# Optimization experiments

Measured on AMD Instinct MI355X. Metric: run time of the kernel, lower is better.

## Reference

```python
import jax, jax.numpy as jnp
import numpy as np

DIM = 128; NH = 4; WS = 7; SS = 3
ZP, HP, WP = 14, 56, 56
NMLP = 512; EPS = 1e-5
N = WS ** 3  # tokens per window (343)


def _ln(x, g, b):
    m = x.mean(-1, keepdims=True)
    v = x.var(-1, keepdims=True)
    return (x - m) / jnp.sqrt(v + EPS) * g + b


def _rel_index():
    # static relative-position index for a cubic (WS,WS,WS) window
    c = np.stack(np.meshgrid(np.arange(WS), np.arange(WS), np.arange(WS), indexing='ij')).reshape(3, -1)
    rel = (c[:, :, None] - c[:, None, :]).transpose(1, 2, 0) + (WS - 1)
    rel[..., 0] *= (2 * WS - 1) ** 2
    rel[..., 1] *= (2 * WS - 1)
    return rel.sum(-1).reshape(-1)  # [N*N]


def _attn_mask():
    # static shifted-window attention mask, [nW, N, N]
    img = np.zeros((ZP, HP, WP), np.float32)
    cnt = 0
    sl = (slice(0, -WS), slice(-WS, -SS), slice(-SS, None))
    for z in sl:
        for h in sl:
            for w in sl:
                img[z, h, w] = cnt
                cnt += 1
    m = img.reshape(ZP // WS, WS, HP // WS, WS, WP // WS, WS)
    m = m.transpose(0, 2, 4, 1, 3, 5).reshape(-1, N)
    d = m[:, None, :] - m[:, :, None]
    return np.where(d != 0, np.float32(-100.0), np.float32(0.0))


_REL_IDX = jnp.asarray(_rel_index())
_MASK = jnp.asarray(_attn_mask())


def setup_inputs() -> dict:
    key = jax.random.key(0)
    ks = jax.random.split(key, 8)
    return {
        'x': jax.random.normal(ks[0], (2, ZP, HP, WP, DIM), jnp.float32),
        'norm1_g': jnp.ones((DIM,), jnp.float32),
        'norm1_b': jnp.zeros((DIM,), jnp.float32),
        'qkv_w': jax.random.normal(ks[1], (DIM, 3 * DIM), jnp.float32) * 0.02,
        'qkv_b': jnp.zeros((3 * DIM,), jnp.float32),
        'rel_table': jax.random.normal(ks[2], ((2 * WS - 1) ** 3, NH), jnp.float32) * 0.02,
        'proj_w': jax.random.normal(ks[3], (DIM, DIM), jnp.float32) * 0.02,
        'proj_b': jnp.zeros((DIM,), jnp.float32),
        'norm2_g': jnp.ones((DIM,), jnp.float32),
        'norm2_b': jnp.zeros((DIM,), jnp.float32),
        'fc1_w': jax.random.normal(ks[4], (DIM, NMLP), jnp.float32) * 0.02,
        'fc1_b': jnp.zeros((NMLP,), jnp.float32),
        'fc2_w': jax.random.normal(ks[5], (NMLP, DIM), jnp.float32) * 0.02,
        'fc2_b': jnp.zeros((DIM,), jnp.float32),
    }


def reference(x, norm1_g, norm1_b, qkv_w, qkv_b, rel_table, proj_w, proj_b,
              norm2_g, norm2_b, fc1_w, fc1_b, fc2_w, fc2_b):
    B, Z, H, W, C = x.shape
    hd = C // NH
    scale = hd ** -0.5
    shortcut = x
    xn = _ln(x, norm1_g, norm1_b)
    # cyclic shift
    xs = jnp.roll(xn, (-SS, -SS, -SS), axis=(1, 2, 3))
    # window partition -> [B*nW, N, C]
    xw = xs.reshape(B, Z // WS, WS, H // WS, WS, W // WS, WS, C)
    xw = xw.transpose(0, 1, 3, 5, 2, 4, 6, 7).reshape(-1, N, C)
    qkv = (xw @ qkv_w + qkv_b).reshape(-1, N, 3, NH, hd).transpose(2, 0, 3, 1, 4)
    q, k, v = qkv[0], qkv[1], qkv[2]  # [Bn, NH, N, hd]
    attn = jnp.einsum('bhnd,bhmd->bhnm', q * scale, k)
    bias = rel_table[_REL_IDX].reshape(N, N, NH).transpose(2, 0, 1)  # [NH, N, N]
    attn = attn + bias[None]
    nW = _MASK.shape[0]
    attn = attn.reshape(B, nW, NH, N, N) + _MASK[None, :, None]
    attn = jax.nn.softmax(attn.reshape(-1, NH, N, N), axis=-1)
    out = jnp.einsum('bhnm,bhmd->bhnd', attn, v)
    out = out.transpose(0, 2, 1, 3).reshape(-1, N, C)
    out = out @ proj_w + proj_b
    # window reverse -> [B, Z, H, W, C]
    out = out.reshape(B, Z // WS, H // WS, W // WS, WS, WS, WS, C)
    out = out.transpose(0, 1, 4, 2, 5, 3, 6, 7).reshape(B, Z, H, W, C)
    out = jnp.roll(out, (SS, SS, SS), axis=(1, 2, 3))
    x1 = shortcut + out
    y = _ln(x1, norm2_g, norm2_b)
    y = jax.nn.gelu(y @ fc1_w + fc1_b, approximate=False) @ fc2_w + fc2_b
    return x1 + y
```

## Files before the change

### kernel.cpp

```cpp
#include <hip/hip_runtime.h>


typedef __attribute__((ext_vector_type(8))) _Float16 half8;
typedef __attribute__((ext_vector_type(4))) _Float16 half4;
typedef __attribute__((ext_vector_type(4))) float floatx4;

#define DEV static __device__ __forceinline__

DEV floatx4 MFMA(half8 a, half8 b, floatx4 c) {
  return __builtin_amdgcn_mfma_f32_16x16x32_f16(a, b, c, 0, 0, 0);
}
DEV floatx4 MFMA16(half4 a, half4 b, floatx4 c) {
  return __builtin_amdgcn_mfma_f32_16x16x16f16(a, b, c, 0, 0, 0);
}

DEV float gelu_f(float v) {
  return v / (1.f + __expf(-1.702f * v));
}

DEV void f4arr(float4 v, float o[4]) {
  o[0] = v.x; o[1] = v.y; o[2] = v.z; o[3] = v.w;
}

DEV void stage_load(half8 pf[8], const _Float16* src, int rst, int tid) {
#pragma unroll
  for (int it = 0; it < 8; ++it) {
    int e = it * 256 + tid;
    int row = e >> 4, seg = e & 15;
    pf[it] = *(const half8*)&src[(size_t)row * rst + seg * 8];
  }
}
DEV void stage_store(_Float16* wb, const half8 pf[8], int tid) {
#pragma unroll
  for (int it = 0; it < 8; ++it) {
    int e = it * 256 + tid;
    int row = e >> 4, seg = e & 15;
    *(half8*)&wb[row * 136 + seg * 8] = pf[it];
  }
}
DEV void stage_tile(_Float16* wb, const _Float16* src, int rst, int tid) {
  half8 pf[8];
  stage_load(pf, src, rst, tid);
  stage_store(wb, pf, tid);
}

__global__ __launch_bounds__(256) void k_prep(
    const float* __restrict__ rel, _Float16* __restrict__ biasH,
    const float* __restrict__ w1, const float* __restrict__ w2,
    const float* __restrict__ wq, const float* __restrict__ wp,
    _Float16* __restrict__ w1h, _Float16* __restrict__ w2h,
    _Float16* __restrict__ wqh, _Float16* __restrict__ wph) {
  int gid = blockIdx.x * 256 + threadIdx.x;
  if (gid < 495616) {
    int reg = gid & 3, quad = (gid >> 2) & 3, ml = (gid >> 4) & 15;
    int u = gid >> 8;
    int nt = u % 22; u /= 22;
    int rt = u % 22; int h = u / 22;
    int q = rt * 16 + ml, kv = nt * 16 + quad * 4 + reg;
    float val = -30000.f;
    if (q < 343 && kv < 343) {
      int lzi = q / 49, ri = q - lzi * 49, lhi = ri / 7, lwi = ri - lhi * 7;
      int lzj = kv / 49, rj = kv - lzj * 49, lhj = rj / 7, lwj = rj - lhj * 7;
      int idx = (lzi - lzj + 6) * 169 + (lhi - lhj + 6) * 13 + (lwi - lwj + 6);
      val = rel[idx * 4 + h];
    }
    biasH[gid] = (_Float16)val;
    return;
  }
  int i = gid - 495616;
  if (i < 65536) {
    int n = i >> 7, k = i & 127;
    w1h[i] = (_Float16)w1[k * 512 + n];
  } else if (i < 131072) {
    int j = i - 65536; int n = j >> 9, k = j & 511;
    w2h[j] = (_Float16)w2[k * 128 + n];
  } else if (i < 180224) {
    int j = i - 131072; int n = j >> 7, k = j & 127;
    wqh[j] = (_Float16)wq[k * 384 + n];
  } else if (i < 196608) {
    int j = i - 180224; int n = j >> 7, k = j & 127;
    wph[j] = (_Float16)wp[k * 128 + n];
  }
}

__global__ __launch_bounds__(256) void k_ln_qkv(
    const float* __restrict__ x, const float* __restrict__ g1,
    const float* __restrict__ b1, const _Float16* __restrict__ wqh,
    const float* __restrict__ bq, _Float16* __restrict__ qkv) {
  __shared__ __align__(16) _Float16 wb[128 * 136];
  const int tid = threadIdx.x, lane = tid & 63, wid = tid >> 6;
  const int ml = lane & 15, quad = lane >> 4;
  const int task = blockIdx.x * 4 + wid;
  const int w = task / 11, pr = task - (task / 11) * 11;
  const int b_ = w >> 7, r = w & 127;
  const int wz = r >> 6, wh = (r >> 3) & 7, ww = r & 7;

  half8 a0[4], a1[4];
#pragma unroll
  for (int hf = 0; hf < 2; ++hf) {
    int t = pr * 32 + hf * 16 + ml; if (t > 342) t = 342;
    int lz = t / 49, rr = t - lz * 49, lh = rr / 7, lw = rr - lh * 7;
    int oz = wz * 7 + lz + 3; if (oz >= 14) oz -= 14;
    int oh = wh * 7 + lh + 3; if (oh >= 56) oh -= 56;
    int ow = ww * 7 + lw + 3; if (ow >= 56) ow -= 56;
    const float* xp = x + ((((b_ * 14 + oz) * 56 + oh) * 56 + ow) << 7);
    float xv[32];
    float s = 0.f, ss = 0.f;
#pragma unroll
    for (int ks = 0; ks < 4; ++ks) {
      float4 p0 = *(const float4*)(xp + ks * 32 + quad * 8);
      float4 p1 = *(const float4*)(xp + ks * 32 + quad * 8 + 4);
      xv[ks * 8 + 0] = p0.x; xv[ks * 8 + 1] = p0.y; xv[ks * 8 + 2] = p0.z; xv[ks * 8 + 3] = p0.w;
      xv[ks * 8 + 4] = p1.x; xv[ks * 8 + 5] = p1.y; xv[ks * 8 + 6] = p1.z; xv[ks * 8 + 7] = p1.w;
      s += (p0.x + p0.y) + (p0.z + p0.w) + (p1.x + p1.y) + (p1.z + p1.w);
      ss += (p0.x * p0.x + p0.y * p0.y) + (p0.z * p0.z + p0.w * p0.w) +
            (p1.x * p1.x + p1.y * p1.y) + (p1.z * p1.z + p1.w * p1.w);
    }
    s += __shfl_xor(s, 16); s += __shfl_xor(s, 32);
    ss += __shfl_xor(ss, 16); ss += __shfl_xor(ss, 32);
    float mean = s * 0.0078125f;
    float rstd = rsqrtf(ss * 0.0078125f - mean * mean + 1e-5f);
#pragma unroll
    for (int ks = 0; ks < 4; ++ks) {
      int k0 = ks * 32 + quad * 8;
      float4 gg0 = *(const float4*)(g1 + k0), gg1 = *(const float4*)(g1 + k0 + 4);
      float4 bb0 = *(const float4*)(b1 + k0), bb1 = *(const float4*)(b1 + k0 + 4);
      half8 a;
      a[0] = (_Float16)((xv[ks * 8 + 0] - mean) * rstd * gg0.x + bb0.x);
      a[1] = (_Float16)((xv[ks * 8 + 1] - mean) * rstd * gg0.y + bb0.y);
      a[2] = (_Float16)((xv[ks * 8 + 2] - mean) * rstd * gg0.z + bb0.z);
      a[3] = (_Float16)((xv[ks * 8 + 3] - mean) * rstd * gg0.w + bb0.w);
      a[4] = (_Float16)((xv[ks * 8 + 4] - mean) * rstd * gg1.x + bb1.x);
      a[5] = (_Float16)((xv[ks * 8 + 5] - mean) * rstd * gg1.y + bb1.y);
      a[6] = (_Float16)((xv[ks * 8 + 6] - mean) * rstd * gg1.z + bb1.z);
      a[7] = (_Float16)((xv[ks * 8 + 7] - mean) * rstd * gg1.w + bb1.w);
      if (hf == 0) a0[ks] = a; else a1[ks] = a;
    }
  }

  const int t0 = pr * 32 + ml;
  const int t1 = t0 + 16;
  _Float16* q0 = qkv + ((size_t)w * 343 + t0) * 384;
  _Float16* q1 = qkv + ((size_t)w * 343 + (t1 < 343 ? t1 : 342)) * 384;

  for (int c = 0; c < 3; ++c) {
    __syncthreads();
    stage_tile(wb, wqh + (size_t)c * 128 * 128, 128, tid);
    __syncthreads();
    for (int ntl = 0; ntl < 8; ++ntl) {
      floatx4 acc0 = {0.f, 0.f, 0.f, 0.f}, acc1 = {0.f, 0.f, 0.f, 0.f};
#pragma unroll
      for (int ks = 0; ks < 4; ++ks) {
        half8 bb = *(const half8*)&wb[(ntl * 16 + ml) * 136 + ks * 32 + quad * 8];
        acc0 = MFMA(bb, a0[ks], acc0);
        acc1 = MFMA(bb, a1[ks], acc1);
      }
      const int colb = c * 128 + ntl * 16 + quad * 4;
      float qb[4]; f4arr(*(const float4*)&bq[colb], qb);
      half4 s0, s1;
#pragma unroll
      for (int reg = 0; reg < 4; ++reg) {
        s0[reg] = (_Float16)(acc0[reg] + qb[reg]);
        s1[reg] = (_Float16)(acc1[reg] + qb[reg]);
      }
      *(half4*)&q0[colb] = s0;
      if (t1 < 343) *(half4*)&q1[colb] = s1;
    }
  }
}

__global__ __launch_bounds__(512, 2) void k_attn(const _Float16* __restrict__ qkv,
                                                 const _Float16* __restrict__ biasH,
                                                 _Float16* __restrict__ aout) {
  __shared__ __align__(16) _Float16 kl[352 * 40];
  __shared__ __align__(16) _Float16 vt[32 * 364];
  __shared__ __align__(16) _Float16 pen[27 * 360];
  __shared__ __align__(4) unsigned char region[352];
  const int tid = threadIdx.x;
  const int w = blockIdx.x >> 2, head = blockIdx.x & 3;
  const int r = w & 127;
  const int wz = r >> 6, wh = (r >> 3) & 7, ww = r & 7;
  const bool fz = (wz == 1), fh = (wh == 7), fw = (ww == 7);

  for (int t = tid; t < 352; t += 512) {
    int rg = 255;
    if (t < 343) {
      int lz = t / 49, rr = t - lz * 49, lh = rr / 7, lw = rr - lh * 7;
      int rz = fz ? (lz < 4 ? 1 : 2) : 0;
      int rh2 = fh ? (lh < 4 ? 1 : 2) : 0;
      int rw2 = fw ? (lw < 4 ? 1 : 2) : 0;
      rg = rz * 9 + rh2 * 3 + rw2;
    }
    region[t] = (unsigned char)rg;
  }
  for (int e = tid; e < 27 * 352; e += 512) {
    int rg = e / 352, t = e - rg * 352;
    int rt_ = 255;
    if (t < 343) {
      int lz = t / 49, rr = t - lz * 49, lh = rr / 7, lw = rr - lh * 7;
      int rz = fz ? (lz < 4 ? 1 : 2) : 0;
      int rh2 = fh ? (lh < 4 ? 1 : 2) : 0;
      int rw2 = fw ? (lw < 4 ? 1 : 2) : 0;
      rt_ = rz * 9 + rh2 * 3 + rw2;
    }
    pen[rg * 360 + t] = (rt_ == rg) ? (_Float16)0.f : (_Float16)(-30000.f);
  }
  const _Float16* qkvw = qkv + (size_t)w * 343 * 384;
  for (int e = tid; e < 352 * 4; e += 512) {
    int t = e >> 2, d8 = (e & 3) * 8;
    half8 v;
    if (t < 343) {
      v = *(const half8*)&qkvw[t * 384 + 128 + head * 32 + d8];
    } else {
#pragma unroll
      for (int j = 0; j < 8; ++j) v[j] = (_Float16)0.f;
    }
    *(half8*)&kl[t * 40 + d8] = v;
  }
  for (int e = tid; e < 343 * 4; e += 512) {
    int t = e >> 2, d8 = (e & 3) * 8;
    half8 v = *(const half8*)&qkvw[t * 384 + 256 + head * 32 + d8];
#pragma unroll
    for (int j = 0; j < 8; ++j) vt[(d8 + j) * 364 + t] = v[j];
  }
  for (int e = tid; e < 9 * 32; e += 512) {
    int t = 343 + (e >> 5), d = e & 31;
    vt[d * 364 + t] = (_Float16)0.f;
  }
  __syncthreads();

  const int lane = tid & 63, wid = tid >> 6;
  const int ml = lane & 15, quad = lane >> 4;
  const float scale = 0.17677669529663687f;

  for (int rt = wid; rt < 22; rt += 8) {
    const int row0 = rt * 16;
    int qrow = row0 + ml; if (qrow > 342) qrow = 342;
    half8 bq8 = *(const half8*)&qkvw[qrow * 384 + head * 32 + quad * 8];
    const int rq = region[qrow];
    const _Float16* penr = &pen[rq * 360 + quad * 4];
    const _Float16* bb = &biasH[(size_t)((head * 22 + rt) * 22) * 256 + ml * 16 + quad * 4];

    floatx4 o0 = {0.f, 0.f, 0.f, 0.f}, o1 = {0.f, 0.f, 0.f, 0.f};
    floatx4 sm4 = {0.f, 0.f, 0.f, 0.f};
#pragma unroll
    for (int g = 0; g < 3; ++g) {
      const int G = (g < 2) ? 8 : 6;
      const int nb = g * 8;
      half4 bp[8];
      floatx4 S[8];
#pragma unroll
      for (int k = 0; k < 8; ++k) if (k < G) {
        half4 b4 = *(const half4*)&bb[(nb + k) * 256];
        half4 p4 = *(const half4*)&penr[(nb + k) * 16];
        bp[k] = b4 + p4;
      }
#pragma unroll
      for (int k = 0; k < 8; ++k) if (k < G) {
        half8 ak = *(const half8*)&kl[((nb + k) * 16 + ml) * 40 + quad * 8];
        S[k] = MFMA(ak, bq8, (floatx4){0.f, 0.f, 0.f, 0.f});
      }
#pragma unroll
      for (int k = 0; k < 8; ++k) if (k < G) {
        half4 p;
#pragma unroll
        for (int reg = 0; reg < 4; ++reg) {
          float v = fmaf(S[k][reg], scale, (float)bp[k][reg]);
          float e = __expf(v);
          sm4[reg] += e;
          p[reg] = (_Float16)e;
        }
        half4 va0 = *(const half4*)&vt[ml * 364 + (nb + k) * 16 + quad * 4];
        half4 va1 = *(const half4*)&vt[(16 + ml) * 364 + (nb + k) * 16 + quad * 4];
        o0 = MFMA16(va0, p, o0);
        o1 = MFMA16(va1, p, o1);
      }
    }
    float sm = (sm4[0] + sm4[1]) + (sm4[2] + sm4[3]);
    sm += __shfl_xor(sm, 16);
    sm += __shfl_xor(sm, 32);

    const int orow = row0 + ml;
    if (orow < 343) {
      float inv = 1.f / sm;
      _Float16* op = aout + ((size_t)w * 343 + orow) * 128 + head * 32;
      half4 s0, s1;
#pragma unroll
      for (int reg = 0; reg < 4; ++reg) {
        s0[reg] = (_Float16)(o0[reg] * inv);
        s1[reg] = (_Float16)(o1[reg] * inv);
      }
      *(half4*)&op[quad * 4] = s0;
      *(half4*)&op[16 + quad * 4] = s1;
    }
  }
}

__global__ __launch_bounds__(256, 2) void k_pm(
    const _Float16* __restrict__ aout, const _Float16* __restrict__ wph,
    const float* __restrict__ bp, const float* __restrict__ x,
    const float* __restrict__ g2, const float* __restrict__ nb2,
    const _Float16* __restrict__ w1h, const float* __restrict__ bfc1,
    const _Float16* __restrict__ w2h, const float* __restrict__ bfc2,
    float* __restrict__ out) {
  __shared__ __align__(16) _Float16 hc[4][32 * 136];
  __shared__ __align__(16) _Float16 wb[128 * 136];
  const int tid = threadIdx.x, lane = tid & 63, wid = tid >> 6;
  const int ml = lane & 15, quad = lane >> 4;
  const int task = blockIdx.x * 4 + wid;
  const int w = task / 11, pr = task - (task / 11) * 11;
  const int b_ = w >> 7, r = w & 127;
  const int wz = r >> 6, wh = (r >> 3) & 7, ww = r & 7;
  const _Float16* ap = aout + (size_t)w * 343 * 128;
  _Float16* hw = &hc[wid][0];

  half8 pf[8];
  stage_load(pf, wph, 128, tid);

  int ra = pr * 32 + ml; if (ra > 342) ra = 342;
  int rbm = pr * 32 + 16 + ml; if (rbm > 342) rbm = 342;
  half8 a0[4], a1[4];
#pragma unroll
  for (int ks = 0; ks < 4; ++ks) {
    a0[ks] = *(const half8*)&ap[ra * 128 + ks * 32 + quad * 8];
    a1[ks] = *(const half8*)&ap[rbm * 128 + ks * 32 + quad * 8];
  }
  int tok[2];
#pragma unroll
  for (int mt = 0; mt < 2; ++mt) {
    int t = pr * 32 + mt * 16 + ml;
    if (t < 343) {
      int lz = t / 49, rr = t - lz * 49, lh = rr / 7, lw = rr - lh * 7;
      int oz = wz * 7 + lz + 3; if (oz >= 14) oz -= 14;
      int oh = wh * 7 + lh + 3; if (oh >= 56) oh -= 56;
      int ow = ww * 7 + lw + 3; if (ow >= 56) ow -= 56;
      tok[mt] = ((b_ * 14 + oz) * 56 + oh) * 56 + ow;
    } else {
      tok[mt] = -1;
    }
  }
  stage_store(wb, pf, tid);
  __syncthreads();
  stage_load(pf, w1h, 128, tid);

  floatx4 px[8][2];
  for (int nt = 0; nt < 8; ++nt) {
    floatx4 acc0 = {0.f, 0.f, 0.f, 0.f}, acc1 = {0.f, 0.f, 0.f, 0.f};
#pragma unroll
    for (int ks = 0; ks < 4; ++ks) {
      half8 bb = *(const half8*)&wb[(nt * 16 + ml) * 136 + ks * 32 + quad * 8];
      acc0 = MFMA(bb, a0[ks], acc0);
      acc1 = MFMA(bb, a1[ks], acc1);
    }
    const int colb = nt * 16 + quad * 4;
    float pb4[4]; f4arr(*(const float4*)&bp[colb], pb4);
    float xr0[4] = {0.f, 0.f, 0.f, 0.f}, xr1[4] = {0.f, 0.f, 0.f, 0.f};
    if (tok[0] >= 0) f4arr(*(const float4*)&x[(size_t)tok[0] * 128 + colb], xr0);
    if (tok[1] >= 0) f4arr(*(const float4*)&x[(size_t)tok[1] * 128 + colb], xr1);
#pragma unroll
    for (int reg = 0; reg < 4; ++reg) {
      px[nt][0][reg] = acc0[reg] + pb4[reg] + xr0[reg];
      px[nt][1][reg] = acc1[reg] + pb4[reg] + xr1[reg];
    }
  }

  float mean[2], rstd[2];
#pragma unroll
  for (int mt = 0; mt < 2; ++mt) {
    float s = 0.f, ss = 0.f;
#pragma unroll
    for (int nt = 0; nt < 8; ++nt)
#pragma unroll
      for (int reg = 0; reg < 4; ++reg) {
        float v = px[nt][mt][reg];
        s += v; ss += v * v;
      }
    s += __shfl_xor(s, 16); s += __shfl_xor(s, 32);
    ss += __shfl_xor(ss, 16); ss += __shfl_xor(ss, 32);
    float m = s * 0.0078125f;
    mean[mt] = m;
    rstd[mt] = rsqrtf(ss * 0.0078125f - m * m + 1e-5f);
  }

  for (int nt = 0; nt < 8; ++nt) {
    const int colb = nt * 16 + quad * 4;
    float g4[4], nb4[4];
    f4arr(*(const float4*)&g2[colb], g4);
    f4arr(*(const float4*)&nb2[colb], nb4);
#pragma unroll
    for (int mt = 0; mt < 2; ++mt) {
      half4 h;
#pragma unroll
      for (int reg = 0; reg < 4; ++reg)
        h[reg] = (_Float16)((px[nt][mt][reg] - mean[mt]) * rstd[mt] * g4[reg] + nb4[reg]);
      *(half4*)&hw[(mt * 16 + ml) * 136 + colb] = h;
    }
  }
  half8 ay[2][4];
#pragma unroll
  for (int mt = 0; mt < 2; ++mt)
#pragma unroll
    for (int ks = 0; ks < 4; ++ks)
      ay[mt][ks] = *(const half8*)&hw[(mt * 16 + ml) * 136 + ks * 32 + quad * 8];

  floatx4 acc2[8][2];
#pragma unroll
  for (int nt = 0; nt < 8; ++nt)
#pragma unroll
    for (int mt = 0; mt < 2; ++mt) acc2[nt][mt] = (floatx4){0.f, 0.f, 0.f, 0.f};

  for (int ch = 0; ch < 4; ++ch) {
    __syncthreads();
    stage_store(wb, pf, tid);
    __syncthreads();
    stage_load(pf, w2h + (size_t)ch * 128, 512, tid);
    for (int nt = 0; nt < 8; ++nt) {
      floatx4 f0 = {0.f, 0.f, 0.f, 0.f}, f1 = {0.f, 0.f, 0.f, 0.f};
#pragma unroll
      for (int ks = 0; ks < 4; ++ks) {
        half8 bb = *(const half8*)&wb[(nt * 16 + ml) * 136 + ks * 32 + quad * 8];
        f0 = MFMA(bb, ay[0][ks], f0);
        f1 = MFMA(bb, ay[1][ks], f1);
      }
      const int colb = nt * 16 + quad * 4;
      float fb4[4]; f4arr(*(const float4*)&bfc1[ch * 128 + colb], fb4);
      half4 h0, h1;
#pragma unroll
      for (int reg = 0; reg < 4; ++reg) {
        h0[reg] = (_Float16)gelu_f(f0[reg] + fb4[reg]);
        h1[reg] = (_Float16)gelu_f(f1[reg] + fb4[reg]);
      }
      *(half4*)&hw[ml * 136 + colb] = h0;
      *(half4*)&hw[(16 + ml) * 136 + colb] = h1;
    }
    __syncthreads();
    stage_store(wb, pf, tid);
    __syncthreads();
    if (ch < 3) stage_load(pf, w1h + (size_t)(ch + 1) * 128 * 128, 128, tid);
#pragma unroll
    for (int ks = 0; ks < 4; ++ks) {
      half8 A0 = *(const half8*)&hw[ml * 136 + ks * 32 + quad * 8];
      half8 A1 = *(const half8*)&hw[(16 + ml) * 136 + ks * 32 + quad * 8];
#pragma unroll
      for (int nt = 0; nt < 8; ++nt) {
        half8 bb = *(const half8*)&wb[(nt * 16 + ml) * 136 + ks * 32 + quad * 8];
        acc2[nt][0] = MFMA(bb, A0, acc2[nt][0]);
        acc2[nt][1] = MFMA(bb, A1, acc2[nt][1]);
      }
    }
  }

  for (int nt = 0; nt < 8; ++nt) {
    const int colb = nt * 16 + quad * 4;
    float fb4[4]; f4arr(*(const float4*)&bfc2[colb], fb4);
#pragma unroll
    for (int mt = 0; mt < 2; ++mt) {
      if (tok[mt] >= 0) {
        float4 o;
        o.x = px[nt][mt][0] + acc2[nt][mt][0] + fb4[0];
        o.y = px[nt][mt][1] + acc2[nt][mt][1] + fb4[1];
        o.z = px[nt][mt][2] + acc2[nt][mt][2] + fb4[2];
        o.w = px[nt][mt][3] + acc2[nt][mt][3] + fb4[3];
        *(float4*)&out[(size_t)tok[mt] * 128 + colb] = o;
      }
    }
  }
}

extern "C" void kernel_launch(void* const* d_in, const int* in_sizes, int n_in,
                              void* d_out, int out_size, void* d_ws, size_t ws_size,
                              hipStream_t stream) {
  (void)in_sizes; (void)n_in; (void)out_size; (void)ws_size;
  const float* x   = (const float*)d_in[0];
  const float* g1  = (const float*)d_in[1];
  const float* b1  = (const float*)d_in[2];
  const float* wq  = (const float*)d_in[3];
  const float* bq  = (const float*)d_in[4];
  const float* rel = (const float*)d_in[5];
  const float* wp  = (const float*)d_in[6];
  const float* bp  = (const float*)d_in[7];
  const float* g2  = (const float*)d_in[8];
  const float* b2_ = (const float*)d_in[9];
  const float* w1  = (const float*)d_in[10];
  const float* bf1 = (const float*)d_in[11];
  const float* w2  = (const float*)d_in[12];
  const float* bf2 = (const float*)d_in[13];

  char* ws = (char*)d_ws;
  _Float16* qkv   = (_Float16*)(ws);
  _Float16* aout  = (_Float16*)(ws + 67436544);
  _Float16* biasH = (_Float16*)(ws + 89915392);
  _Float16* w1h   = (_Float16*)(ws + 91897856);
  _Float16* w2h   = (_Float16*)(ws + 92028928);
  _Float16* wqh   = (_Float16*)(ws + 92160000);
  _Float16* wph   = (_Float16*)(ws + 92258304);
  float*    out   = (float*)d_out;

  hipLaunchKernelGGL(k_prep,   dim3(2704), dim3(256), 0, stream,
                     rel, biasH, w1, w2, wq, wp, w1h, w2h, wqh, wph);
  hipLaunchKernelGGL(k_ln_qkv, dim3(704),  dim3(256), 0, stream, x, g1, b1, wqh, bq, qkv);
  hipLaunchKernelGGL(k_attn,   dim3(1024), dim3(512), 0, stream, qkv, biasH, aout);
  hipLaunchKernelGGL(k_pm,     dim3(704),  dim3(256), 0, stream,
                     aout, wph, bp, x, g2, b2_, w1h, bf1, w2h, bf2, out);
}
```

Measured before the change: 281.5 us.

## Shrink k_pm per-wave tile to 16 rows with 8 waves per block

The projection+MLP kernel now runs 512-thread blocks with 8 waves, each handling 16 token rows instead of 32, while the grid size stays the same. Halving per-wave accumulators and register tiles lowers register pressure and raises the number of waves per CU, and each staged weight tile in shared memory is reused by more waves. The trade-off is fewer MFMAs per B-fragment LDS read, which lowers arithmetic intensity per wave, and larger blocks that must synchronise at each barrier.

Result: slower. 289.0 us (+2.6%).

```diff
diff --git a/kernel.cpp b/kernel.cpp
--- a/kernel.cpp
+++ b/kernel.cpp
@@ -42,6 +42,22 @@
   half8 pf[8];
   stage_load(pf, src, rst, tid);
   stage_store(wb, pf, tid);
+}
+DEV void stage_load5(half8 pf[4], const _Float16* src, int rst, int tid) {
+#pragma unroll
+  for (int it = 0; it < 4; ++it) {
+    int e = it * 512 + tid;
+    int row = e >> 4, seg = e & 15;
+    pf[it] = *(const half8*)&src[(size_t)row * rst + seg * 8];
+  }
+}
+DEV void stage_store5(_Float16* wb, const half8 pf[4], int tid) {
+#pragma unroll
+  for (int it = 0; it < 4; ++it) {
+    int e = it * 512 + tid;
+    int row = e >> 4, seg = e & 15;
+    *(half8*)&wb[row * 136 + seg * 8] = pf[it];
+  }
 }
 
 __global__ __launch_bounds__(256) void k_prep(
@@ -296,90 +312,81 @@
   }
 }
 
-__global__ __launch_bounds__(256, 2) void k_pm(
+__global__ __launch_bounds__(512, 2) void k_pm(
     const _Float16* __restrict__ aout, const _Float16* __restrict__ wph,
     const float* __restrict__ bp, const float* __restrict__ x,
     const float* __restrict__ g2, const float* __restrict__ nb2,
     const _Float16* __restrict__ w1h, const float* __restrict__ bfc1,
     const _Float16* __restrict__ w2h, const float* __restrict__ bfc2,
     float* __restrict__ out) {
-  __shared__ __align__(16) _Float16 hc[4][32 * 136];
+  __shared__ __align__(16) _Float16 hc[8][16 * 136];
   __shared__ __align__(16) _Float16 wb[128 * 136];
   const int tid = threadIdx.x, lane = tid & 63, wid = tid >> 6;
   const int ml = lane & 15, quad = lane >> 4;
-  const int task = blockIdx.x * 4 + wid;
-  const int w = task / 11, pr = task - (task / 11) * 11;
+  const int task = blockIdx.x * 8 + wid;
+  const int w = task / 22, tk = task - (task / 22) * 22;
   const int b_ = w >> 7, r = w & 127;
   const int wz = r >> 6, wh = (r >> 3) & 7, ww = r & 7;
   const _Float16* ap = aout + (size_t)w * 343 * 128;
   _Float16* hw = &hc[wid][0];
 
-  half8 pf[8];
-  stage_load(pf, wph, 128, tid);
-
-  int ra = pr * 32 + ml; if (ra > 342) ra = 342;
-  int rbm = pr * 32 + 16 + ml; if (rbm > 342) rbm = 342;
-  half8 a0[4], a1[4];
-#pragma unroll
-  for (int ks = 0; ks < 4; ++ks) {
+  half8 pf[4];
+  stage_load5(pf, wph, 128, tid);
+
+  int ra = tk * 16 + ml; if (ra > 342) ra = 342;
+  half8 a0[4];
+#pragma unroll
+  for (int ks = 0; ks < 4; ++ks)
     a0[ks] = *(const half8*)&ap[ra * 128 + ks * 32 + quad * 8];
-    a1[ks] = *(const half8*)&ap[rbm * 128 + ks * 32 + quad * 8];
-  }
-  int tok[2];
-#pragma unroll
-  for (int mt = 0; mt < 2; ++mt) {
-    int t = pr * 32 + mt * 16 + ml;
+
+  int tok;
+  {
+    int t = tk * 16 + ml;
     if (t < 343) {
       int lz = t / 49, rr = t - lz * 49, lh = rr / 7, lw = rr - lh * 7;
       int oz = wz * 7 + lz + 3; if (oz >= 14) oz -= 14;
       int oh = wh * 7 + lh + 3; if (oh >= 56) oh -= 56;
       int ow = ww * 7 + lw + 3; if (ow >= 56) ow -= 56;
-      tok[mt] = ((b_ * 14 + oz) * 56 + oh) * 56 + ow;
+      tok = ((b_ * 14 + oz) * 56 + oh) * 56 + ow;
     } else {
-      tok[mt] = -1;
-    }
-  }
-  stage_store(wb, pf, tid);
+      tok = -1;
+    }
+  }
+  stage_store5(wb, pf, tid);
   __syncthreads();
-  stage_load(pf, w1h, 128, tid);
-
-  floatx4 px[8][2];
+  stage_load5(pf, w1h, 128, tid);
+
+  floatx4 px[8];
   for (int nt = 0; nt < 8; ++nt) {
-    floatx4 acc0 = {0.f, 0.f, 0.f, 0.f}, acc1 = {0.f, 0.f, 0.f, 0.f};
+    floatx4 acc = {0.f, 0.f, 0.f, 0.f};
 #pragma unroll
     for (int ks = 0; ks < 4; ++ks) {
       half8 bb = *(const half8*)&wb[(nt * 16 + ml) * 136 + ks * 32 + quad * 8];
-      acc0 = MFMA(bb, a0[ks], acc0);
-      acc1 = MFMA(bb, a1[ks], acc1);
+      acc = MFMA(bb, a0[ks], acc);
     }
     const int colb = nt * 16 + quad * 4;
     float pb4[4]; f4arr(*(const float4*)&bp[colb], pb4);
-    float xr0[4] = {0.f, 0.f, 0.f, 0.f}, xr1[4] = {0.f, 0.f, 0.f, 0.f};
-    if (tok[0] >= 0) f4arr(*(const float4*)&x[(size_t)tok[0] * 128 + colb], xr0);
-    if (tok[1] >= 0) f4arr(*(const float4*)&x[(size_t)tok[1] * 128 + colb], xr1);
-#pragma unroll
-    for (int reg = 0; reg < 4; ++reg) {
-      px[nt][0][reg] = acc0[reg] + pb4[reg] + xr0[reg];
-      px[nt][1][reg] = acc1[reg] + pb4[reg] + xr1[reg];
-    }
-  }
-
-  float mean[2], rstd[2];
-#pragma unroll
-  for (int mt = 0; mt < 2; ++mt) {
+    float xr[4] = {0.f, 0.f, 0.f, 0.f};
+    if (tok >= 0) f4arr(*(const float4*)&x[(size_t)tok * 128 + colb], xr);
+#pragma unroll
+    for (int reg = 0; reg < 4; ++reg)
+      px[nt][reg] = acc[reg] + pb4[reg] + xr[reg];
+  }
+
+  float mean, rstd;
+  {
     float s = 0.f, ss = 0.f;
 #pragma unroll
     for (int nt = 0; nt < 8; ++nt)
 #pragma unroll
       for (int reg = 0; reg < 4; ++reg) {
-        float v = px[nt][mt][reg];
+        float v = px[nt][reg];
         s += v; ss += v * v;
       }
     s += __shfl_xor(s, 16); s += __shfl_xor(s, 32);
     ss += __shfl_xor(ss, 16); ss += __shfl_xor(ss, 32);
-    float m = s * 0.0078125f;
-    mean[mt] = m;
-    rstd[mt] = rsqrtf(ss * 0.0078125f - m * m + 1e-5f);
+    mean = s * 0.0078125f;
+    rstd = rsqrtf(ss * 0.0078125f - mean * mean + 1e-5f);
   }
 
   for (int nt = 0; nt < 8; ++nt) {
@@ -387,82 +394,66 @@
     float g4[4], nb4[4];
     f4arr(*(const float4*)&g2[colb], g4);
     f4arr(*(const float4*)&nb2[colb], nb4);
-#pragma unroll
-    for (int mt = 0; mt < 2; ++mt) {
-      half4 h;
-#pragma unroll
-      for (int reg = 0; reg < 4; ++reg)
-        h[reg] = (_Float16)((px[nt][mt][reg] - mean[mt]) * rstd[mt] * g4[reg] + nb4[reg]);
-      *(half4*)&hw[(mt * 16 + ml) * 136 + colb] = h;
-    }
-  }
-  half8 ay[2][4];
-#pragma unroll
-  for (int mt = 0; mt < 2; ++mt)
-#pragma unroll
-    for (int ks = 0; ks < 4; ++ks)
-      ay[mt][ks] = *(const half8*)&hw[(mt * 16 + ml) * 136 + ks * 32 + quad * 8];
-
-  floatx4 acc2[8][2];
-#pragma unroll
-  for (int nt = 0; nt < 8; ++nt)
-#pragma unroll
-    for (int mt = 0; mt < 2; ++mt) acc2[nt][mt] = (floatx4){0.f, 0.f, 0.f, 0.f};
+    half4 h;
+#pragma unroll
+    for (int reg = 0; reg < 4; ++reg)
+      h[reg] = (_Float16)((px[nt][reg] - mean) * rstd * g4[reg] + nb4[reg]);
+    *(half4*)&hw[ml * 136 + colb] = h;
+  }
+  half8 ay[4];
+#pragma unroll
+  for (int ks = 0; ks < 4; ++ks)
+    ay[ks] = *(const half8*)&hw[ml * 136 + ks * 32 + quad * 8];
+
+  floatx4 acc2[8];
+#pragma unroll
+  for (int nt = 0; nt < 8; ++nt) acc2[nt] = (floatx4){0.f, 0.f, 0.f, 0.f};
 
   for (int ch = 0; ch < 4; ++ch) {
     __syncthreads();
-    stage_store(wb, pf, tid);
-    __syncthreads();
-    stage_load(pf, w2h + (size_t)ch * 128, 512, tid);
+    stage_store5(wb, pf, tid);
+    __syncthreads();
+    stage_load5(pf, w2h + (size_t)ch * 128, 512, tid);
     for (int nt = 0; nt < 8; ++nt) {
-      floatx4 f0 = {0.f, 0.f, 0.f, 0.f}, f1 = {0.f, 0.f, 0.f, 0.f};
+      floatx4 f0 = {0.f, 0.f, 0.f, 0.f};
 #pragma unroll
       for (int ks = 0; ks < 4; ++ks) {
         half8 bb = *(const half8*)&wb[(nt * 16 + ml) * 136 + ks * 32 + quad * 8];
-        f0 = MFMA(bb, ay[0][ks], f0);
-        f1 = MFMA(bb, ay[1][ks], f1);
+        f0 = MFMA(bb, ay[ks], f0);
       }
       const int colb = nt * 16 + quad * 4;
       float fb4[4]; f4arr(*(const float4*)&bfc1[ch * 128 + colb], fb4);
-      half4 h0, h1;
-#pragma unroll
-      for (int reg = 0; reg < 4; ++reg) {
+      half4 h0;
+#pragma unroll
+      for (int reg = 0; reg < 4; ++reg)
         h0[reg] = (_Float16)gelu_f(f0[reg] + fb4[reg]);
-        h1[reg] = (_Float16)gelu_f(f1[reg] + fb4[reg]);
-      }
       *(half4*)&hw[ml * 136 + colb] = h0;
-      *(half4*)&hw[(16 + ml) * 136 + colb] = h1;
-    }
-    __syncthreads();
-    stage_store(wb, pf, tid);
-    __syncthreads();
-    if (ch < 3) stage_load(pf, w1h + (size_t)(ch + 1) * 128 * 128, 128, tid);
+    }
+    __syncthreads();
+    stage_store5(wb, pf, tid);
+    __syncthreads();
+    if (ch < 3) stage_load5(pf, w1h + (size_t)(ch + 1) * 128 * 128, 128, tid);
 #pragma unroll
     for (int ks = 0; ks < 4; ++ks) {
       half8 A0 = *(const half8*)&hw[ml * 136 + ks * 32 + quad * 8];
-      half8 A1 = *(const half8*)&hw[(16 + ml) * 136 + ks * 32 + quad * 8];
 #pragma unroll
       for (int nt = 0; nt < 8; ++nt) {
         half8 bb = *(const half8*)&wb[(nt * 16 + ml) * 136 + ks * 32 + quad * 8];
-        acc2[nt][0] = MFMA(bb, A0, acc2[nt][0]);
-        acc2[nt][1] = MFMA(bb, A1, acc2[nt][1]);
-      }
-    }
-  }
-
-  for (int nt = 0; nt < 8; ++nt) {
-    const int colb = nt * 16 + quad * 4;
-    float fb4[4]; f4arr(*(const float4*)&bfc2[colb], fb4);
-#pragma unroll
-    for (int mt = 0; mt < 2; ++mt) {
-      if (tok[mt] >= 0) {
-        float4 o;
-        o.x = px[nt][mt][0] + acc2[nt][mt][0] + fb4[0];
-        o.y = px[nt][mt][1] + acc2[nt][mt][1] + fb4[1];
-        o.z = px[nt][mt][2] + acc2[nt][mt][2] + fb4[2];
-        o.w = px[nt][mt][3] + acc2[nt][mt][3] + fb4[3];
-        *(float4*)&out[(size_t)tok[mt] * 128 + colb] = o;
-      }
+        acc2[nt] = MFMA(bb, A0, acc2[nt]);
+      }
+    }
+  }
+
+  if (tok >= 0) {
+    for (int nt = 0; nt < 8; ++nt) {
+      const int colb = nt * 16 + quad * 4;
+      float fb4[4]; f4arr(*(const float4*)&bfc2[colb], fb4);
+      float4 o;
+      o.x = px[nt][0] + acc2[nt][0] + fb4[0];
+      o.y = px[nt][1] + acc2[nt][1] + fb4[1];
+      o.z = px[nt][2] + acc2[nt][2] + fb4[2];
+      o.w = px[nt][3] + acc2[nt][3] + fb4[3];
+      *(float4*)&out[(size_t)tok * 128 + colb] = o;
     }
   }
 }
@@ -500,6 +491,6 @@
                      rel, biasH, w1, w2, wq, wp, w1h, w2h, wqh, wph);
   hipLaunchKernelGGL(k_ln_qkv, dim3(704),  dim3(256), 0, stream, x, g1, b1, wqh, bq, qkv);
   hipLaunchKernelGGL(k_attn,   dim3(1024), dim3(512), 0, stream, qkv, biasH, aout);
-  hipLaunchKernelGGL(k_pm,     dim3(704),  dim3(256), 0, stream,
+  hipLaunchKernelGGL(k_pm,     dim3(704),  dim3(512), 0, stream,
                      aout, wph, bp, x, g2, b2_, w1h, bf1, w2h, bf2, out);
 }
```
